# Kernel tuning notes

Measured on AMD Instinct MI355X. Metric: run time of the kernel, lower is better.

## Reference

```python
import jax, jax.numpy as jnp
import numpy as np

B, S, D, E, K = 4, 4096, 2048, 64, 2


def setup_inputs() -> dict:
    key = jax.random.key(0)
    kx, kwg, kwn, kn = jax.random.split(key, 4)
    scale = 1.0 / np.sqrt(D)
    return {
        "x": jax.random.normal(kx, (B, S, D), dtype=jnp.float32),
        "Wg": jax.random.normal(kwg, (E, D), dtype=jnp.float32) * scale,
        "bg": jnp.zeros((E,), dtype=jnp.float32),
        "Wn": jax.random.normal(kwn, (E, D), dtype=jnp.float32) * scale,
        "bn": jnp.zeros((E,), dtype=jnp.float32),
        "noise": jax.random.normal(kn, (B, S, E), dtype=jnp.float32),
    }


def reference(x, Wg, bg, Wn, bn, noise):
    # gate / noise projections: [B,S,D] @ [D,E] -> [B,S,E]
    gate_logits = jnp.einsum("bsd,ed->bse", x, Wg) + bg
    noise_std = jax.nn.softplus(jnp.einsum("bsd,ed->bse", x, Wn) + bn)
    noisy_logits = gate_logits + noise * noise_std  # training-mode path

    # top-k over experts, then scatter back with -inf elsewhere
    flat = noisy_logits.reshape(-1, E)  # [T, E], T = B*S
    top_vals, top_idx = jax.lax.top_k(flat, K)  # [T, K]
    T = flat.shape[0]
    neg_inf = jnp.full((T, E), -jnp.inf, dtype=flat.dtype)
    full_logits = neg_inf.at[jnp.arange(T)[:, None], top_idx].set(top_vals)

    gate_probs = jax.nn.softmax(full_logits, axis=-1).reshape(B, S, E)
    top_k_indices = top_idx.reshape(B, S, K)
    return gate_probs, top_k_indices
```

## Files before the change

### kernel.cpp

```cpp
#include <hip/hip_runtime.h>
#include <math.h>
#include <stdint.h>

#define D_ 2048
#define E_ 64
#define T_ 16384

#define BM 32
#define BK 64
#define KTILES 32
#define ABUF_B 8192
#define BBUF_B 32768
#define BUF_B (ABUF_B + BBUF_B)
#define CT_STRIDE 132

typedef _Float16 h8 __attribute__((ext_vector_type(8)));
typedef float f4v __attribute__((ext_vector_type(4)));

__device__ __forceinline__ void split2(const float4& a, const float4& b,
                                       h8& h, h8& m) {
    const float xe[8] = {a.x, a.y, a.z, a.w, b.x, b.y, b.z, b.w};
#pragma unroll
    for (int i = 0; i < 8; ++i) {
        const _Float16 hh_ = (_Float16)xe[i];
        const float r = (xe[i] - (float)hh_) * 1024.0f;
        h[i] = hh_;
        m[i] = (_Float16)r;
    }
}

__device__ __forceinline__ void gload16(const void* g, void* l) {
    __builtin_amdgcn_global_load_lds(
        (const __attribute__((address_space(1))) uint32_t*)g,
        (__attribute__((address_space(3))) uint32_t*)l, 16, 0, 0);
}

__device__ __forceinline__ void topk_epilogue(float g, float nl, float nz,
                                              int lane, size_t tg,
                                              float* __restrict__ out_probs,
                                              float* __restrict__ out_idx) {
    const float sp = fmaxf(nl, 0.f) + log1pf(expf(-fabsf(nl)));
    const float noisy = g + nz * sp;

    float v = noisy;
    int idx = lane;
#pragma unroll
    for (int off = 32; off > 0; off >>= 1) {
        const float ov = __shfl_xor(v, off);
        const int oi = __shfl_xor(idx, off);
        if (ov > v || (ov == v && oi < idx)) { v = ov; idx = oi; }
    }
    const float v1 = v;
    const int i1 = idx;
    v = (lane == i1) ? -INFINITY : noisy;
    idx = lane;
#pragma unroll
    for (int off = 32; off > 0; off >>= 1) {
        const float ov = __shfl_xor(v, off);
        const int oi = __shfl_xor(idx, off);
        if (ov > v || (ov == v && oi < idx)) { v = ov; idx = oi; }
    }
    const float v2 = v;
    const int i2 = idx;

    const float e2 = expf(v2 - v1);
    const float denom = 1.f + e2;
    const float p = (lane == i1) ? (1.f / denom)
                                 : ((lane == i2) ? (e2 / denom) : 0.f);
    out_probs[tg * E_ + lane] = p;
    if (lane == 0) {
        out_idx[tg * 2 + 0] = (float)i1;
        out_idx[tg * 2 + 1] = (float)i2;
    }
}

__global__ void w_split_kernel(const float* __restrict__ Wg,
                               const float* __restrict__ Wn,
                               h8* __restrict__ wsp) {
    const int idx = blockIdx.x * blockDim.x + threadIdx.x;
    const int lane = idx & 63;
    const int s = (idx >> 6) & 63;
    const int f = idx >> 12;
    const int n = f * 16 + (lane & 15);
    const int k0 = s * 32 + ((lane >> 4) << 3);
    const float* src = (n < 64) ? &Wg[(size_t)n * D_ + k0]
                                : &Wn[(size_t)(n - 64) * D_ + k0];
    h8 hv, mv;
#pragma unroll
    for (int i = 0; i < 8; ++i) {
        const float w = src[i];
        const _Float16 wh = (_Float16)w;
        const float r = (w - (float)wh) * 1024.0f;
        hv[i] = wh;
        mv[i] = (_Float16)r;
    }
    wsp[0 * 32768 + idx] = hv;
    wsp[1 * 32768 + idx] = mv;
}

__launch_bounds__(512, 4)
__global__ void gemm_topk_kernel(const float* __restrict__ x,
                                 const h8* __restrict__ wsp,
                                 const float* __restrict__ bg,
                                 const float* __restrict__ bn,
                                 const float* __restrict__ noise,
                                 float* __restrict__ out_probs,
                                 float* __restrict__ out_idx) {
    __shared__ __align__(16) char smem[2 * BUF_B];
    const int tid = threadIdx.x;
    const int lane = tid & 63;
    const int wv = tid >> 6;
    const int wm = wv >> 2;
    const int wn = wv & 3;
    const int block_m0 = blockIdx.x * BM;
    const char* wb = (const char*)wsp;

    const int sfrag = (tid >> 7) & 1;
    const int sks = (tid >> 6) & 1;
    const int sl = tid & 63;
    const int srow = sfrag * 16 + (sl & 15);
    const int schunk = sks * 4 + (sl >> 4);
    const float* asrc = x + (size_t)(block_m0 + srow) * D_ + schunk * 8;
    const int aw_hi = ((0 * 2 + sfrag) * 2 + sks) * 1024 + sl * 16;
    const int aw_mid = ((1 * 2 + sfrag) * 2 + sks) * 1024 + sl * 16;

    f4v hh[2] = {}, cx[2] = {}, mm[2] = {};

    auto STAGE_B = [&](int t, int b) {
        char* Bb = smem + b * BUF_B + ABUF_B;
#pragma unroll
        for (int p = 0; p < 2; ++p)
#pragma unroll
            for (int ks = 0; ks < 2; ++ks)
                gload16(wb + ((size_t)(p * 32768 + wv * 4096 + (t * 2 + ks) * 64 + lane)) * 16,
                        Bb + ((p * 8 + wv) * 2 + ks) * 1024 + lane * 16);
    };
    auto ALOAD = [&](int t, float4& ra, float4& rb) {
        if (tid < 256) {
            ra = *(const float4*)(asrc + t * BK);
            rb = *(const float4*)(asrc + t * BK + 4);
        }
    };
    auto ASPLIT = [&](const float4& ra, const float4& rb, int b) {
        if (tid < 256) {
            h8 hv, mv;
            split2(ra, rb, hv, mv);
            char* Ab = smem + b * BUF_B;
            *(h8*)(Ab + aw_hi) = hv;
            *(h8*)(Ab + aw_mid) = mv;
        }
    };
    auto COMPUTE = [&](int b) {
        const char* Ab = smem + b * BUF_B;
        const char* Bb = Ab + ABUF_B;
#pragma unroll
        for (int ks = 0; ks < 2; ++ks) {
            h8 ah, am, bh[2], bm[2];
            ah = *(const h8*)(Ab + ((0 * 2 + wm) * 2 + ks) * 1024 + lane * 16);
            am = *(const h8*)(Ab + ((1 * 2 + wm) * 2 + ks) * 1024 + lane * 16);
#pragma unroll
            for (int nf = 0; nf < 2; ++nf) {
                const int f = wn * 2 + nf;
                bh[nf] = *(const h8*)(Bb + ((0 * 8 + f) * 2 + ks) * 1024 + lane * 16);
                bm[nf] = *(const h8*)(Bb + ((1 * 8 + f) * 2 + ks) * 1024 + lane * 16);
            }
#define MF(A, B, C) C = __builtin_amdgcn_mfma_f32_16x16x32_f16(A, B, C, 0, 0, 0)
#pragma unroll
            for (int nf = 0; nf < 2; ++nf) {
                MF(ah, bh[nf], hh[nf]);
                MF(ah, bm[nf], cx[nf]);
                MF(am, bh[nf], cx[nf]);
                MF(am, bm[nf], mm[nf]);
            }
#undef MF
        }
    };

    float4 ra0{}, rb0{}, ra1{}, rb1{};
    ALOAD(0, ra0, rb0);
    STAGE_B(0, 0);
    ASPLIT(ra0, rb0, 0);
    ALOAD(1, ra0, rb0);
    __syncthreads();

#pragma unroll 1
    for (int i = 0; i < KTILES / 2; ++i) {
        const int t = 2 * i;
        STAGE_B(t + 1, 1);
        if (t + 2 < KTILES) ALOAD(t + 2, ra1, rb1);
        COMPUTE(0);
        ASPLIT(ra0, rb0, 1);
        __syncthreads();
        if (t + 2 < KTILES) STAGE_B(t + 2, 0);
        if (t + 3 < KTILES) ALOAD(t + 3, ra0, rb0);
        COMPUTE(1);
        if (t + 2 < KTILES) ASPLIT(ra1, rb1, 0);
        __syncthreads();
    }

    float* Ct = (float*)smem;
    {
        const float S1 = 1.0f / 1024.0f;
        const float S2 = S1 * S1;
        const int arow = lane & 15;
        const int ko4 = (lane >> 4) * 4;
#pragma unroll
        for (int nf = 0; nf < 2; ++nf) {
            const int col = wn * 32 + nf * 16 + arow;
#pragma unroll
            for (int r = 0; r < 4; ++r) {
                const int row = wm * 16 + ko4 + r;
                Ct[row * CT_STRIDE + col] =
                    hh[nf][r] + cx[nf][r] * S1 + mm[nf][r] * S2;
            }
        }
    }
    __syncthreads();

    const float my_bg = bg[lane];
    const float my_bn = bn[lane];
#pragma unroll 1
    for (int tt = 0; tt < 4; ++tt) {
        const int tl = wv * 4 + tt;
        const size_t tg = (size_t)block_m0 + tl;
        const float g = Ct[tl * CT_STRIDE + lane] + my_bg;
        const float nl = Ct[tl * CT_STRIDE + 64 + lane] + my_bn;
        const float nz = noise[tg * E_ + lane];
        topk_epilogue(g, nl, nz, lane, tg, out_probs, out_idx);
    }
}

#define FBM 64
#define FBK 32
#define XS_STRIDE 68
#define WS_STRIDE 132
#define FCT_STRIDE 132

__launch_bounds__(256)
__global__ void noisy_topk_f32_kernel(const float* __restrict__ x,
                                      const float* __restrict__ Wg,
                                      const float* __restrict__ bg,
                                      const float* __restrict__ Wn,
                                      const float* __restrict__ bn,
                                      const float* __restrict__ noise,
                                      float* __restrict__ out_probs,
                                      float* __restrict__ out_idx) {
    __shared__ float smem[FBM * FCT_STRIDE];
    float* Xs = smem;
    float* Ws = smem + FBK * XS_STRIDE;

    const int tid = threadIdx.x;
    const int block_m0 = blockIdx.x * FBM;
    const int n0 = (tid & 31) * 4;
    const int m0 = (tid >> 5) * 8;

    float acc[8][4];
#pragma unroll
    for (int i = 0; i < 8; ++i)
#pragma unroll
        for (int j = 0; j < 4; ++j) acc[i][j] = 0.f;

    const int sj = tid & 7;
    const int sr = tid >> 3;

    for (int k0 = 0; k0 < D_; k0 += FBK) {
        __syncthreads();
#pragma unroll
        for (int it = 0; it < 2; ++it) {
            const int m = sr + it * 32;
            const float4 v = *reinterpret_cast<const float4*>(
                &x[(size_t)(block_m0 + m) * D_ + k0 + 4 * sj]);
            Xs[(4 * sj + 0) * XS_STRIDE + m] = v.x;
            Xs[(4 * sj + 1) * XS_STRIDE + m] = v.y;
            Xs[(4 * sj + 2) * XS_STRIDE + m] = v.z;
            Xs[(4 * sj + 3) * XS_STRIDE + m] = v.w;
        }
#pragma unroll
        for (int it = 0; it < 4; ++it) {
            const int n = sr + it * 32;
            const float* wrow = (n < 64) ? &Wg[(size_t)n * D_] : &Wn[(size_t)(n - 64) * D_];
            const float4 v = *reinterpret_cast<const float4*>(&wrow[k0 + 4 * sj]);
            Ws[(4 * sj + 0) * WS_STRIDE + n] = v.x;
            Ws[(4 * sj + 1) * WS_STRIDE + n] = v.y;
            Ws[(4 * sj + 2) * WS_STRIDE + n] = v.z;
            Ws[(4 * sj + 3) * WS_STRIDE + n] = v.w;
        }
        __syncthreads();
#pragma unroll
        for (int k = 0; k < FBK; ++k) {
            const float4 a0 = *reinterpret_cast<const float4*>(&Xs[k * XS_STRIDE + m0]);
            const float4 a1 = *reinterpret_cast<const float4*>(&Xs[k * XS_STRIDE + m0 + 4]);
            const float4 b4 = *reinterpret_cast<const float4*>(&Ws[k * WS_STRIDE + n0]);
            const float am[8] = {a0.x, a0.y, a0.z, a0.w, a1.x, a1.y, a1.z, a1.w};
            const float bb[4] = {b4.x, b4.y, b4.z, b4.w};
#pragma unroll
            for (int i = 0; i < 8; ++i)
#pragma unroll
                for (int j = 0; j < 4; ++j)
                    acc[i][j] = fmaf(am[i], bb[j], acc[i][j]);
        }
    }

    __syncthreads();
    float* Ct = smem;
#pragma unroll
    for (int i = 0; i < 8; ++i)
#pragma unroll
        for (int j = 0; j < 4; ++j)
            Ct[(m0 + i) * FCT_STRIDE + n0 + j] = acc[i][j];
    __syncthreads();

    const int wave = tid >> 6;
    const int lane = tid & 63;
    const float my_bg = bg[lane];
    const float my_bn = bn[lane];
#pragma unroll 1
    for (int tt = 0; tt < 16; ++tt) {
        const int tl = wave * 16 + tt;
        const size_t tg = (size_t)block_m0 + tl;
        const float g = Ct[tl * FCT_STRIDE + lane] + my_bg;
        const float nl = Ct[tl * FCT_STRIDE + 64 + lane] + my_bn;
        const float nz = noise[tg * E_ + lane];
        topk_epilogue(g, nl, nz, lane, tg, out_probs, out_idx);
    }
}

extern "C" void kernel_launch(void* const* d_in, const int* in_sizes, int n_in,
                              void* d_out, int out_size, void* d_ws, size_t ws_size,
                              hipStream_t stream) {
    const float* x = (const float*)d_in[0];
    const float* Wg = (const float*)d_in[1];
    const float* bg = (const float*)d_in[2];
    const float* Wn = (const float*)d_in[3];
    const float* bn = (const float*)d_in[4];
    const float* noise = (const float*)d_in[5];
    float* out_probs = (float*)d_out;
    float* out_idx = out_probs + (size_t)T_ * E_;

    const size_t WSP_BYTES = (size_t)2 * 32768 * 16;
    if (ws_size >= WSP_BYTES) {
        h8* wsp = (h8*)d_ws;
        hipLaunchKernelGGL(w_split_kernel, dim3(128), dim3(256), 0, stream, Wg, Wn, wsp);
        hipLaunchKernelGGL(gemm_topk_kernel, dim3(T_ / BM), dim3(512), 0, stream,
                           x, wsp, bg, bn, noise, out_probs, out_idx);
    } else {
        hipLaunchKernelGGL(noisy_topk_f32_kernel, dim3(T_ / FBM), dim3(256), 0, stream,
                           x, Wg, bg, Wn, bn, noise, out_probs, out_idx);
    }
}
```

Before: 61.11 us.

## Double K-chunk per stage and drop the mid*mid split-precision MFMA term

New measurement: 75.27 us. +23.2%, slower.

```diff
diff --git a/kernel.cpp b/kernel.cpp
--- a/kernel.cpp
+++ b/kernel.cpp
@@ -7,10 +7,10 @@
 #define T_ 16384
 
 #define BM 32
-#define BK 64
-#define KTILES 32
-#define ABUF_B 8192
-#define BBUF_B 32768
+#define CHUNK 128
+#define NCHUNK 16
+#define ABUF_B 16384
+#define BBUF_B 65536
 #define BUF_B (ABUF_B + BBUF_B)
 #define CT_STRIDE 132
 
@@ -98,7 +98,7 @@
     wsp[1 * 32768 + idx] = mv;
 }
 
-__launch_bounds__(512, 4)
+__launch_bounds__(512)
 __global__ void gemm_topk_kernel(const float* __restrict__ x,
                                  const h8* __restrict__ wsp,
                                  const float* __restrict__ bg,
@@ -115,54 +115,50 @@
     const int block_m0 = blockIdx.x * BM;
     const char* wb = (const char*)wsp;
 
-    const int sfrag = (tid >> 7) & 1;
-    const int sks = (tid >> 6) & 1;
+    const int smf = tid >> 8;
+    const int sks = (tid >> 6) & 3;
     const int sl = tid & 63;
-    const int srow = sfrag * 16 + (sl & 15);
-    const int schunk = sks * 4 + (sl >> 4);
-    const float* asrc = x + (size_t)(block_m0 + srow) * D_ + schunk * 8;
-    const int aw_hi = ((0 * 2 + sfrag) * 2 + sks) * 1024 + sl * 16;
-    const int aw_mid = ((1 * 2 + sfrag) * 2 + sks) * 1024 + sl * 16;
-
-    f4v hh[2] = {}, cx[2] = {}, mm[2] = {};
+    const int srow = smf * 16 + (sl & 15);
+    const float* asrc = x + (size_t)(block_m0 + srow) * D_ + ((sl >> 4) << 3);
+    const int aw_hi = ((0 * 2 + smf) * 4 + sks) * 1024 + sl * 16;
+    const int aw_mid = ((1 * 2 + smf) * 4 + sks) * 1024 + sl * 16;
+    const int asrc_off = sks * 32;
+
+    f4v hh[2] = {}, cx[2] = {};
 
     auto STAGE_B = [&](int t, int b) {
         char* Bb = smem + b * BUF_B + ABUF_B;
 #pragma unroll
         for (int p = 0; p < 2; ++p)
 #pragma unroll
-            for (int ks = 0; ks < 2; ++ks)
-                gload16(wb + ((size_t)(p * 32768 + wv * 4096 + (t * 2 + ks) * 64 + lane)) * 16,
-                        Bb + ((p * 8 + wv) * 2 + ks) * 1024 + lane * 16);
+            for (int ks = 0; ks < 4; ++ks)
+                gload16(wb + ((size_t)(p * 32768 + wv * 4096 + (t * 4 + ks) * 64 + lane)) * 16,
+                        Bb + ((p * 8 + wv) * 4 + ks) * 1024 + lane * 16);
     };
     auto ALOAD = [&](int t, float4& ra, float4& rb) {
-        if (tid < 256) {
-            ra = *(const float4*)(asrc + t * BK);
-            rb = *(const float4*)(asrc + t * BK + 4);
-        }
+        ra = *(const float4*)(asrc + t * CHUNK + asrc_off);
+        rb = *(const float4*)(asrc + t * CHUNK + asrc_off + 4);
     };
     auto ASPLIT = [&](const float4& ra, const float4& rb, int b) {
-        if (tid < 256) {
-            h8 hv, mv;
-            split2(ra, rb, hv, mv);
-            char* Ab = smem + b * BUF_B;
-            *(h8*)(Ab + aw_hi) = hv;
-            *(h8*)(Ab + aw_mid) = mv;
-        }
+        h8 hv, mv;
+        split2(ra, rb, hv, mv);
+        char* Ab = smem + b * BUF_B;
+        *(h8*)(Ab + aw_hi) = hv;
+        *(h8*)(Ab + aw_mid) = mv;
     };
     auto COMPUTE = [&](int b) {
         const char* Ab = smem + b * BUF_B;
         const char* Bb = Ab + ABUF_B;
 #pragma unroll
-        for (int ks = 0; ks < 2; ++ks) {
+        for (int ks = 0; ks < 4; ++ks) {
             h8 ah, am, bh[2], bm[2];
-            ah = *(const h8*)(Ab + ((0 * 2 + wm) * 2 + ks) * 1024 + lane * 16);
-            am = *(const h8*)(Ab + ((1 * 2 + wm) * 2 + ks) * 1024 + lane * 16);
+            ah = *(const h8*)(Ab + ((0 * 2 + wm) * 4 + ks) * 1024 + lane * 16);
+            am = *(const h8*)(Ab + ((1 * 2 + wm) * 4 + ks) * 1024 + lane * 16);
 #pragma unroll
             for (int nf = 0; nf < 2; ++nf) {
                 const int f = wn * 2 + nf;
-                bh[nf] = *(const h8*)(Bb + ((0 * 8 + f) * 2 + ks) * 1024 + lane * 16);
-                bm[nf] = *(const h8*)(Bb + ((1 * 8 + f) * 2 + ks) * 1024 + lane * 16);
+                bh[nf] = *(const h8*)(Bb + ((0 * 8 + f) * 4 + ks) * 1024 + lane * 16);
+                bm[nf] = *(const h8*)(Bb + ((1 * 8 + f) * 4 + ks) * 1024 + lane * 16);
             }
 #define MF(A, B, C) C = __builtin_amdgcn_mfma_f32_16x16x32_f16(A, B, C, 0, 0, 0)
 #pragma unroll
@@ -170,13 +166,12 @@
                 MF(ah, bh[nf], hh[nf]);
                 MF(ah, bm[nf], cx[nf]);
                 MF(am, bh[nf], cx[nf]);
-                MF(am, bm[nf], mm[nf]);
             }
 #undef MF
         }
     };
 
-    float4 ra0{}, rb0{}, ra1{}, rb1{};
+    float4 ra0, rb0, ra1, rb1;
     ALOAD(0, ra0, rb0);
     STAGE_B(0, 0);
     ASPLIT(ra0, rb0, 0);
@@ -184,24 +179,23 @@
     __syncthreads();
 
 #pragma unroll 1
-    for (int i = 0; i < KTILES / 2; ++i) {
+    for (int i = 0; i < NCHUNK / 2; ++i) {
         const int t = 2 * i;
         STAGE_B(t + 1, 1);
-        if (t + 2 < KTILES) ALOAD(t + 2, ra1, rb1);
+        if (t + 2 < NCHUNK) ALOAD(t + 2, ra1, rb1);
         COMPUTE(0);
         ASPLIT(ra0, rb0, 1);
         __syncthreads();
-        if (t + 2 < KTILES) STAGE_B(t + 2, 0);
-        if (t + 3 < KTILES) ALOAD(t + 3, ra0, rb0);
+        if (t + 2 < NCHUNK) STAGE_B(t + 2, 0);
+        if (t + 3 < NCHUNK) ALOAD(t + 3, ra0, rb0);
         COMPUTE(1);
-        if (t + 2 < KTILES) ASPLIT(ra1, rb1, 0);
+        if (t + 2 < NCHUNK) ASPLIT(ra1, rb1, 0);
         __syncthreads();
     }
 
     float* Ct = (float*)smem;
     {
         const float S1 = 1.0f / 1024.0f;
-        const float S2 = S1 * S1;
         const int arow = lane & 15;
         const int ko4 = (lane >> 4) * 4;
 #pragma unroll
@@ -210,8 +204,7 @@
 #pragma unroll
             for (int r = 0; r < 4; ++r) {
                 const int row = wm * 16 + ko4 + r;
-                Ct[row * CT_STRIDE + col] =
-                    hh[nf][r] + cx[nf][r] * S1 + mm[nf][r] * S2;
+                Ct[row * CT_STRIDE + col] = hh[nf][r] + cx[nf][r] * S1;
             }
         }
     }
```

## Switch to 32x32x16 MFMA with split-K across warps and drop mid*mid term

Applied to the files above, without the earlier changes.

New measurement: 61.12 us. About the same (+0.0%).

```diff
diff --git a/kernel.cpp b/kernel.cpp
--- a/kernel.cpp
+++ b/kernel.cpp
@@ -8,14 +8,14 @@
 
 #define BM 32
 #define BK 64
-#define KTILES 32
+#define NT 32
 #define ABUF_B 8192
 #define BBUF_B 32768
 #define BUF_B (ABUF_B + BBUF_B)
 #define CT_STRIDE 132
 
 typedef _Float16 h8 __attribute__((ext_vector_type(8)));
-typedef float f4v __attribute__((ext_vector_type(4)));
+typedef float f16v __attribute__((ext_vector_type(16)));
 
 __device__ __forceinline__ void split2(const float4& a, const float4& b,
                                        h8& h, h8& m) {
@@ -79,10 +79,10 @@
                                h8* __restrict__ wsp) {
     const int idx = blockIdx.x * blockDim.x + threadIdx.x;
     const int lane = idx & 63;
-    const int s = (idx >> 6) & 63;
-    const int f = idx >> 12;
-    const int n = f * 16 + (lane & 15);
-    const int k0 = s * 32 + ((lane >> 4) << 3);
+    const int s = (idx >> 6) & 127;
+    const int f = idx >> 13;
+    const int n = f * 32 + (lane & 31);
+    const int k0 = s * 16 + ((lane >> 5) << 3);
     const float* src = (n < 64) ? &Wg[(size_t)n * D_ + k0]
                                 : &Wn[(size_t)(n - 64) * D_ + k0];
     h8 hv, mv;
@@ -98,7 +98,7 @@
     wsp[1 * 32768 + idx] = mv;
 }
 
-__launch_bounds__(512, 4)
+__launch_bounds__(512)
 __global__ void gemm_topk_kernel(const float* __restrict__ x,
                                  const h8* __restrict__ wsp,
                                  const float* __restrict__ bg,
@@ -110,30 +110,29 @@
     const int tid = threadIdx.x;
     const int lane = tid & 63;
     const int wv = tid >> 6;
-    const int wm = wv >> 2;
+    const int kh = wv >> 2;
     const int wn = wv & 3;
     const int block_m0 = blockIdx.x * BM;
     const char* wb = (const char*)wsp;
 
-    const int sfrag = (tid >> 7) & 1;
-    const int sks = (tid >> 6) & 1;
+    const int ks_s = tid >> 6;
     const int sl = tid & 63;
-    const int srow = sfrag * 16 + (sl & 15);
-    const int schunk = sks * 4 + (sl >> 4);
-    const float* asrc = x + (size_t)(block_m0 + srow) * D_ + schunk * 8;
-    const int aw_hi = ((0 * 2 + sfrag) * 2 + sks) * 1024 + sl * 16;
-    const int aw_mid = ((1 * 2 + sfrag) * 2 + sks) * 1024 + sl * 16;
-
-    f4v hh[2] = {}, cx[2] = {}, mm[2] = {};
+    const float* asrc = x + (size_t)(block_m0 + (sl & 31)) * D_
+                          + (ks_s & 3) * 16 + ((sl >> 5) << 3);
+    const int aw_hi = (0 * 4 + (ks_s & 3)) * 1024 + sl * 16;
+    const int aw_mid = (1 * 4 + (ks_s & 3)) * 1024 + sl * 16;
+
+    f16v hh = {}, cx = {};
 
     auto STAGE_B = [&](int t, int b) {
         char* Bb = smem + b * BUF_B + ABUF_B;
 #pragma unroll
-        for (int p = 0; p < 2; ++p)
-#pragma unroll
-            for (int ks = 0; ks < 2; ++ks)
-                gload16(wb + ((size_t)(p * 32768 + wv * 4096 + (t * 2 + ks) * 64 + lane)) * 16,
-                        Bb + ((p * 8 + wv) * 2 + ks) * 1024 + lane * 16);
+        for (int j = 0; j < 4; ++j) {
+            const int rid = wv * 4 + j;
+            const int p = rid >> 4, f = (rid & 15) >> 2, ks = rid & 3;
+            gload16(wb + ((size_t)(p * 32768 + f * 8192 + (t * 4 + ks) * 64 + lane)) * 16,
+                    Bb + rid * 1024 + lane * 16);
+        }
     };
     auto ALOAD = [&](int t, float4& ra, float4& rb) {
         if (tid < 256) {
@@ -154,25 +153,15 @@
         const char* Ab = smem + b * BUF_B;
         const char* Bb = Ab + ABUF_B;
 #pragma unroll
-        for (int ks = 0; ks < 2; ++ks) {
-            h8 ah, am, bh[2], bm[2];
-            ah = *(const h8*)(Ab + ((0 * 2 + wm) * 2 + ks) * 1024 + lane * 16);
-            am = *(const h8*)(Ab + ((1 * 2 + wm) * 2 + ks) * 1024 + lane * 16);
-#pragma unroll
-            for (int nf = 0; nf < 2; ++nf) {
-                const int f = wn * 2 + nf;
-                bh[nf] = *(const h8*)(Bb + ((0 * 8 + f) * 2 + ks) * 1024 + lane * 16);
-                bm[nf] = *(const h8*)(Bb + ((1 * 8 + f) * 2 + ks) * 1024 + lane * 16);
-            }
-#define MF(A, B, C) C = __builtin_amdgcn_mfma_f32_16x16x32_f16(A, B, C, 0, 0, 0)
-#pragma unroll
-            for (int nf = 0; nf < 2; ++nf) {
-                MF(ah, bh[nf], hh[nf]);
-                MF(ah, bm[nf], cx[nf]);
-                MF(am, bh[nf], cx[nf]);
-                MF(am, bm[nf], mm[nf]);
-            }
-#undef MF
+        for (int ksl = 0; ksl < 2; ++ksl) {
+            const int ks = kh * 2 + ksl;
+            const h8 ah = *(const h8*)(Ab + (0 * 4 + ks) * 1024 + lane * 16);
+            const h8 am = *(const h8*)(Ab + (1 * 4 + ks) * 1024 + lane * 16);
+            const h8 bh = *(const h8*)(Bb + ((0 * 16 + wn * 4 + ks)) * 1024 + lane * 16);
+            const h8 bm = *(const h8*)(Bb + ((1 * 16 + wn * 4 + ks)) * 1024 + lane * 16);
+            hh = __builtin_amdgcn_mfma_f32_32x32x16_f16(ah, bh, hh, 0, 0, 0);
+            cx = __builtin_amdgcn_mfma_f32_32x32x16_f16(ah, bm, cx, 0, 0, 0);
+            cx = __builtin_amdgcn_mfma_f32_32x32x16_f16(am, bh, cx, 0, 0, 0);
         }
     };
 
@@ -184,38 +173,42 @@
     __syncthreads();
 
 #pragma unroll 1
-    for (int i = 0; i < KTILES / 2; ++i) {
+    for (int i = 0; i < NT / 2; ++i) {
         const int t = 2 * i;
         STAGE_B(t + 1, 1);
-        if (t + 2 < KTILES) ALOAD(t + 2, ra1, rb1);
+        if (t + 2 < NT) ALOAD(t + 2, ra1, rb1);
         COMPUTE(0);
         ASPLIT(ra0, rb0, 1);
         __syncthreads();
-        if (t + 2 < KTILES) STAGE_B(t + 2, 0);
-        if (t + 3 < KTILES) ALOAD(t + 3, ra0, rb0);
+        if (t + 2 < NT) STAGE_B(t + 2, 0);
+        if (t + 3 < NT) ALOAD(t + 3, ra0, rb0);
         COMPUTE(1);
-        if (t + 2 < KTILES) ASPLIT(ra1, rb1, 0);
+        if (t + 2 < NT) ASPLIT(ra1, rb1, 0);
         __syncthreads();
     }
 
     float* Ct = (float*)smem;
     {
         const float S1 = 1.0f / 1024.0f;
-        const float S2 = S1 * S1;
-        const int arow = lane & 15;
-        const int ko4 = (lane >> 4) * 4;
-#pragma unroll
-        for (int nf = 0; nf < 2; ++nf) {
-            const int col = wn * 32 + nf * 16 + arow;
-#pragma unroll
-            for (int r = 0; r < 4; ++r) {
-                const int row = wm * 16 + ko4 + r;
-                Ct[row * CT_STRIDE + col] =
-                    hh[nf][r] + cx[nf][r] * S1 + mm[nf][r] * S2;
+        const int col = wn * 32 + (lane & 31);
+        const int rbase = 4 * (lane >> 5);
+        if (kh == 0) {
+#pragma unroll
+            for (int r = 0; r < 16; ++r) {
+                const int row = (r & 3) + 8 * (r >> 2) + rbase;
+                Ct[row * CT_STRIDE + col] = hh[r] + cx[r] * S1;
             }
         }
-    }
-    __syncthreads();
+        __syncthreads();
+        if (kh == 1) {
+#pragma unroll
+            for (int r = 0; r < 16; ++r) {
+                const int row = (r & 3) + 8 * (r >> 2) + rbase;
+                Ct[row * CT_STRIDE + col] += hh[r] + cx[r] * S1;
+            }
+        }
+        __syncthreads();
+    }
 
     const float my_bg = bg[lane];
     const float my_bn = bn[lane];
```
